# Optimization experiments

Hardware: AMD Instinct MI355X
Metric: run time of the kernel (lower is better)

Reference implementation:

```python
import jax, jax.numpy as jnp
import numpy as np

N = 1500                 # number of proposals
NUM_CLASSES = 81         # COCO: background + 80
NMS_THRESH = 0.5
SCORE_THRESH = 0.05
MAX_DET = 100            # config.test.max_det
BBOX_REG_WEIGHTS = jnp.array([10.0, 10.0, 5.0, 5.0], dtype=jnp.float32)


def setup_inputs() -> dict:
    key = jax.random.key(0)
    k1, k2, k3 = jax.random.split(key, 3)
    H, W = 800.0, 1333.0
    # realistic proposals: random centers / sizes inside the image
    cx = jax.random.uniform(jax.random.fold_in(k1, 0), (N,)) * W
    cy = jax.random.uniform(jax.random.fold_in(k1, 1), (N,)) * H
    bw = jax.random.uniform(jax.random.fold_in(k1, 2), (N,)) * 200.0 + 16.0
    bh = jax.random.uniform(jax.random.fold_in(k1, 3), (N,)) * 200.0 + 16.0
    bottom_rois = jnp.stack(
        [jnp.zeros((N,)), cx - 0.5 * bw, cy - 0.5 * bh, cx + 0.5 * bw, cy + 0.5 * bh],
        axis=1).astype(jnp.float32)
    bbox_delta = (jax.random.normal(k2, (N, 4 * NUM_CLASSES)) * 0.5).astype(jnp.float32)
    cls_prob = jax.nn.softmax(jax.random.normal(k3, (N, NUM_CLASSES)) * 2.0, axis=-1).astype(jnp.float32)
    im_info = jnp.array([[H, W, 1.0]], dtype=jnp.float32)
    return {"bottom_rois": bottom_rois, "bbox_delta": bbox_delta,
            "cls_prob": cls_prob, "im_info": im_info}


def _decode_boxes(rois, deltas, im_info):
    # rois [N,4], deltas [N,4C] -> clipped boxes [N,C,4] (legacy +1 convention)
    x1, y1, x2, y2 = rois[:, 0], rois[:, 1], rois[:, 2], rois[:, 3]
    w = x2 - x1 + 1.0
    h = y2 - y1 + 1.0
    cx = x1 + 0.5 * w
    cy = y1 + 0.5 * h
    d = deltas.reshape(deltas.shape[0], -1, 4) / BBOX_REG_WEIGHTS  # [N,C,4]
    pcx = cx[:, None] + w[:, None] * d[..., 0]
    pcy = cy[:, None] + h[:, None] * d[..., 1]
    pw = w[:, None] * jnp.exp(d[..., 2])
    ph = h[:, None] * jnp.exp(d[..., 3])
    boxes = jnp.stack([pcx - 0.5 * pw, pcy - 0.5 * ph,
                       pcx + 0.5 * pw - 1.0, pcy + 0.5 * ph - 1.0], axis=-1)
    hw = im_info[0, :2]  # [height, width]
    lim = jnp.stack([hw[1] - 1.0, hw[0] - 1.0, hw[1] - 1.0, hw[0] - 1.0])
    return jnp.clip(boxes, 0.0, lim)


def _pairwise_iou(b):
    # b [N,4], legacy +1 areas (matches gpu_nms)
    x1, y1, x2, y2 = b[:, 0], b[:, 1], b[:, 2], b[:, 3]
    area = (x2 - x1 + 1.0) * (y2 - y1 + 1.0)
    iw = jnp.maximum(jnp.minimum(x2[:, None], x2[None, :]) - jnp.maximum(x1[:, None], x1[None, :]) + 1.0, 0.0)
    ih = jnp.maximum(jnp.minimum(y2[:, None], y2[None, :]) - jnp.maximum(y1[:, None], y1[None, :]) + 1.0, 0.0)
    inter = iw * ih
    return inter / (area[:, None] + area[None, :] - inter)


def _nms_one_class(boxes, scores):
    # boxes [N,4], scores [N] -> score-sorted boxes/scores + keep mask
    valid = scores > SCORE_THRESH
    order = jnp.argsort(-scores)
    b = boxes[order]
    s = scores[order]
    v = valid[order]
    iou = jax.lax.stop_gradient(_pairwise_iou(b))  # used only in comparisons

    def body(suppressed, i):
        keep_i = v[i] & ~suppressed[i]
        suppressed = suppressed | (keep_i & (iou[i] > NMS_THRESH))
        return suppressed, keep_i

    _, keep = jax.lax.scan(body, jnp.zeros((b.shape[0],), bool), jnp.arange(b.shape[0]))
    return b, s, keep


def reference(bottom_rois, bbox_delta, cls_prob, im_info):
    boxes = _decode_boxes(bottom_rois[:, 1:], bbox_delta, im_info)  # [N,C,4]
    C = cls_prob.shape[1]
    boxes_fg = jnp.swapaxes(boxes, 0, 1)[1:]   # [C-1,N,4]
    scores_fg = cls_prob.T[1:]                 # [C-1,N]
    b, s, keep = jax.vmap(_nms_one_class)(boxes_fg, scores_fg)
    # image-level max_det cap (>= kth score, as in source)
    flat = jnp.where(keep, s, -jnp.inf).reshape(-1)
    n_keep = keep.sum()
    kth = jax.lax.top_k(flat, MAX_DET)[0][-1]
    keep = keep & jnp.where(n_keep > MAX_DET, s >= kth, True)
    cls_idx = jnp.broadcast_to(jnp.arange(1, C)[:, None], s.shape)
    zeros = jnp.zeros_like(s[..., None])
    dets = jnp.concatenate([zeros, b, s[..., None]], axis=-1)  # [C-1,N,6]
    dets = jnp.where(keep[..., None], dets, 0.0).reshape(-1, 6)
    return dets, cls_idx.reshape(-1), keep.reshape(-1)
```

## Files before the change

kernel.cpp:

```cpp
#include <hip/hip_runtime.h>
#include <math.h>

#pragma clang fp contract(off)

#define N_ROIS     1500
#define NUM_CLS    81
#define FG         80
#define MAXC       1536
#define NMS_T      0.5f
#define SCORE_T    0.05f
#define MAX_DET    100
#define TOTAL      (FG * N_ROIS)
#define TPB        256
#define LDS_STAGE  12288

__device__ __forceinline__ unsigned f2s(float f) {
    unsigned u = __float_as_uint(f);
    return (u & 0x80000000u) ? ~u : (u | 0x80000000u);
}
__device__ __forceinline__ float s2f(unsigned u) {
    return __uint_as_float((u & 0x80000000u) ? (u & 0x7FFFFFFFu) : ~u);
}

__global__ __launch_bounds__(TPB) void nms_kernel(
    const float* __restrict__ rois,
    const float* __restrict__ deltas,
    const float* __restrict__ prob,
    const float* __restrict__ iminfo,
    float4* __restrict__ keptBox,
    int*    __restrict__ keptRow,
    float*  __restrict__ keptScore,
    int*    __restrict__ counter,
    float*  __restrict__ out)
{
    __shared__ unsigned long long key[MAXC];
    __shared__ unsigned long long skey[MAXC];
    __shared__ float4 box4[MAXC];
    __shared__ unsigned char keepf[MAXC], supp[MAXC];
    __shared__ int mcnt;

    const int tid = threadIdx.x;
    const int c = blockIdx.x + 1;
    const int cbase = blockIdx.x * N_ROIS;

    if (tid == 0) mcnt = 0;
    __syncthreads();

    for (int i = tid; i < N_ROIS; i += TPB) {
        float s = prob[i * NUM_CLS + c];
        if (s > SCORE_T) {
            int p = atomicAdd(&mcnt, 1);
            key[p] = ((unsigned long long)(~f2s(s)) << 32) | (unsigned)i;
        }
    }

    {
        const float4 z4 = make_float4(0.f, 0.f, 0.f, 0.f);
        float4* dets4 = (float4*)(out + (size_t)cbase * 6);
        for (int i = tid; i < N_ROIS * 6 / 4; i += TPB) dets4[i] = z4;
        const float fc = (float)c;
        const float4 c4 = make_float4(fc, fc, fc, fc);
        float4* cls4  = (float4*)(out + (size_t)TOTAL * 6 + cbase);
        float4* keep4 = (float4*)(out + (size_t)TOTAL * 7 + cbase);
        for (int i = tid; i < N_ROIS / 4; i += TPB) { cls4[i] = c4; keep4[i] = z4; }
    }
    __syncthreads();
    const int M = mcnt;
    if (M == 0) return;

    for (int i = tid; i < M; i += TPB) {
        unsigned long long kk = key[i];
        int cnt = 0;
        #pragma unroll 4
        for (int j = 0; j < M; ++j) cnt += (int)(key[j] < kk);
        skey[cnt] = kk;
    }
    __syncthreads();

    const float Hm1 = iminfo[0] - 1.0f;
    const float Wm1 = iminfo[1] - 1.0f;
    for (int k = tid; k < M; k += TPB) {
        unsigned long long kk = skey[k];
        int i = (int)(kk & 0xFFFFFFFFu);
        const float* rp = rois + i * 5;
        float x1 = rp[1], y1 = rp[2], x2 = rp[3], y2 = rp[4];
        float w  = x2 - x1 + 1.0f;
        float h  = y2 - y1 + 1.0f;
        float cx = x1 + 0.5f * w;
        float cy = y1 + 0.5f * h;
        const float* dp = deltas + i * (4 * NUM_CLS) + c * 4;
        float dx = dp[0] / 10.0f, dy = dp[1] / 10.0f;
        float dw = dp[2] / 5.0f,  dh = dp[3] / 5.0f;
        float pcx = cx + w * dx;
        float pcy = cy + h * dy;
        float pw  = w * expf(dw);
        float ph  = h * expf(dh);
        float a1 = pcx - 0.5f * pw;
        float a2 = pcy - 0.5f * ph;
        float a3 = pcx + 0.5f * pw - 1.0f;
        float a4 = pcy + 0.5f * ph - 1.0f;
        a1 = fminf(fmaxf(a1, 0.0f), Wm1);
        a2 = fminf(fmaxf(a2, 0.0f), Hm1);
        a3 = fminf(fmaxf(a3, 0.0f), Wm1);
        a4 = fminf(fmaxf(a4, 0.0f), Hm1);
        box4[k] = make_float4(a1, a2, a3, a4);
        keepf[k] = 0; supp[k] = 0;
    }
    __syncthreads();

    const int MW = (M + 63) >> 6;
    const bool fast = (M * MW <= MAXC);

    if (fast) {
        const int wave = tid >> 6, lane = tid & 63;
        for (int r = wave; r < M; r += TPB / 64) {
            float4 br = box4[r];
            float ar = (br.z - br.x + 1.0f) * (br.w - br.y + 1.0f);
            for (int w = 0; w < MW; ++w) {
                int col = (w << 6) | lane;
                int j = col < M ? col : M - 1;
                float4 bj = box4[j];
                float aj = (bj.z - bj.x + 1.0f) * (bj.w - bj.y + 1.0f);
                float iw = fminf(br.z, bj.z) - fmaxf(br.x, bj.x) + 1.0f;
                float ih = fminf(br.w, bj.w) - fmaxf(br.y, bj.y) + 1.0f;
                iw = fmaxf(iw, 0.0f);
                ih = fmaxf(ih, 0.0f);
                float inter = iw * ih;
                float iou = inter / ((ar + aj) - inter);
                bool pred = (col > r) && (col < M) && (iou > NMS_T);
                unsigned long long m = __ballot(pred);
                if (lane == 0) key[r * MW + w] = m;
            }
        }
        __syncthreads();

        if (tid < 64) {
            const int lw = (tid < MW) ? tid : 0;
            unsigned long long acc = 0;
            for (int k = 0; k < M; ++k) {
                unsigned long long m = key[k * MW + lw];
                int bit = (int)((acc >> (k & 63)) & 1ull);
                int sup = __shfl(bit, k >> 6, 64);
                if (!sup) {
                    acc |= m;
                    if (tid == 0) keepf[k] = 1;
                }
            }
        }
        __syncthreads();
    } else {
        for (int k = 0; k < M; ++k) {
            if (!supp[k]) {
                if (tid == 0) keepf[k] = 1;
                float4 bk = box4[k];
                float ak = (bk.z - bk.x + 1.0f) * (bk.w - bk.y + 1.0f);
                for (int j = k + 1 + tid; j < M; j += TPB) {
                    float4 bj = box4[j];
                    float aj = (bj.z - bj.x + 1.0f) * (bj.w - bj.y + 1.0f);
                    float iw = fminf(bk.z, bj.z) - fmaxf(bk.x, bj.x) + 1.0f;
                    float ih = fminf(bk.w, bj.w) - fmaxf(bk.y, bj.y) + 1.0f;
                    iw = fmaxf(iw, 0.0f);
                    ih = fmaxf(ih, 0.0f);
                    float inter = iw * ih;
                    float iou = inter / ((ak + aj) - inter);
                    if (iou > NMS_T) supp[j] = 1;
                }
            }
            __syncthreads();
        }
    }

    for (int k = tid; k < M; k += TPB) {
        if (keepf[k]) {
            int p = atomicAdd(counter, 1);
            keptRow[p]   = cbase + k;
            keptBox[p]   = box4[k];
            keptScore[p] = s2f(~(unsigned)(skey[k] >> 32));
        }
    }
}

__global__ __launch_bounds__(1024) void topk_scatter(
    const int*    __restrict__ counter,
    const int*    __restrict__ keptRow,
    const float4* __restrict__ keptBox,
    const float*  __restrict__ keptScore,
    float* __restrict__ out)
{
    __shared__ unsigned sbits[LDS_STAGE];
    __shared__ int hist[256];
    __shared__ int gsum[64];
    __shared__ unsigned s_pref;
    __shared__ int s_kk;

    const int tid = threadIdx.x;
    const int n = *counter;
    const bool filt = (n > MAX_DET);
    float kth = -INFINITY;

    if (filt) {
        const bool useLds = (n <= LDS_STAGE);
        if (useLds)
            for (int i = tid; i < n; i += 1024) sbits[i] = f2s(keptScore[i]);
        if (tid == 0) { s_pref = 0u; s_kk = MAX_DET; }
        __syncthreads();
        for (int d = 0; d < 4; ++d) {
            const int shift = 24 - 8 * d;
            if (tid < 256) hist[tid] = 0;
            __syncthreads();
            const unsigned pref = s_pref;
            for (int i = tid; i < n; i += 1024) {
                unsigned u = useLds ? sbits[i] : f2s(keptScore[i]);
                if (d == 0 || (u >> (shift + 8)) == pref)
                    atomicAdd(&hist[(u >> shift) & 255u], 1);
            }
            __syncthreads();
            if (tid < 64) {
                int g = tid;
                gsum[g] = hist[4*g] + hist[4*g+1] + hist[4*g+2] + hist[4*g+3];
            }
            if (tid == 0) {
                int kk = s_kk;
                int acc = 0;
                int g = 63;
                for (; g > 0; --g) {
                    int gs = gsum[g];
                    if (acc + gs >= kk) break;
                    acc += gs;
                }
                int v = 4 * g + 3;
                for (; v > 4 * g; --v) {
                    int h = hist[v];
                    if (acc + h >= kk) break;
                    acc += h;
                }
                s_pref = (pref << 8) | (unsigned)v;
                s_kk = kk - acc;
            }
            __syncthreads();
        }
        kth = s2f(s_pref);
    }

    for (int i = tid; i < n; i += 1024) {
        float s = keptScore[i];
        if (!filt || s >= kth) {
            int r = keptRow[i];
            float4 b4 = keptBox[i];
            float* dst = out + (size_t)r * 6;
            dst[1] = b4.x; dst[2] = b4.y; dst[3] = b4.z; dst[4] = b4.w; dst[5] = s;
            out[(size_t)TOTAL * 7 + r] = 1.0f;
        }
    }
}

extern "C" void kernel_launch(void* const* d_in, const int* in_sizes, int n_in,
                              void* d_out, int out_size, void* d_ws, size_t ws_size,
                              hipStream_t stream) {
    const float* rois   = (const float*)d_in[0];
    const float* deltas = (const float*)d_in[1];
    const float* prob   = (const float*)d_in[2];
    const float* iminfo = (const float*)d_in[3];
    float* out = (float*)d_out;

    float4* keptBox   = (float4*)d_ws;
    int*    keptRow   = (int*)(keptBox + TOTAL);
    float*  keptScore = (float*)(keptRow + TOTAL);
    int*    counter   = (int*)(keptScore + TOTAL);

    hipMemsetAsync(counter, 0, sizeof(int), stream);
    nms_kernel<<<FG, TPB, 0, stream>>>(rois, deltas, prob, iminfo,
                                       keptBox, keptRow, keptScore, counter, out);
    topk_scatter<<<1, 1024, 0, stream>>>(counter, keptRow, keptBox, keptScore, out);
}
```

Before: 108.9 us.

## Fuse top-k scatter into NMS kernel via last-block-done counter

Merges the separate single-block top-k/scatter kernel into the NMS kernel: each block bumps an arrival counter after a threadfence, and the last block to arrive runs the radix-select and scatter with 256 threads, reusing the key LDS buffer for staging. It also compacts the score-threshold filter with wave ballot/popcount so there is one LDS atomic per wave instead of per element, and precomputes box areas in LDS. The aim is to remove a kernel launch and its inter-kernel gap. In exchange the serial tail runs with 4x fewer threads, and a smaller LDS staging limit can push large kept counts onto the global-memory path.

```diff
diff --git a/kernel.cpp b/kernel.cpp
--- a/kernel.cpp
+++ b/kernel.cpp
@@ -12,7 +12,6 @@
 #define MAX_DET    100
 #define TOTAL      (FG * N_ROIS)
 #define TPB        256
-#define LDS_STAGE  12288
 
 __device__ __forceinline__ unsigned f2s(float f) {
     unsigned u = __float_as_uint(f);
@@ -22,7 +21,7 @@
     return __uint_as_float((u & 0x80000000u) ? (u & 0x7FFFFFFFu) : ~u);
 }
 
-__global__ __launch_bounds__(TPB) void nms_kernel(
+__global__ __launch_bounds__(TPB) void nms_fused(
     const float* __restrict__ rois,
     const float* __restrict__ deltas,
     const float* __restrict__ prob,
@@ -30,27 +29,40 @@
     float4* __restrict__ keptBox,
     int*    __restrict__ keptRow,
     float*  __restrict__ keptScore,
-    int*    __restrict__ counter,
+    int*    __restrict__ ctrs,
     float*  __restrict__ out)
 {
     __shared__ unsigned long long key[MAXC];
     __shared__ unsigned long long skey[MAXC];
     __shared__ float4 box4[MAXC];
+    __shared__ float  areaA[MAXC];
     __shared__ unsigned char keepf[MAXC], supp[MAXC];
-    __shared__ int mcnt;
-
-    const int tid = threadIdx.x;
+    __shared__ int hist[256];
+    __shared__ int gsum[64];
+    __shared__ unsigned s_pref;
+    __shared__ int s_kk;
+    __shared__ int mcnt, s_arr;
+
+    const int tid  = threadIdx.x;
+    const int lane = tid & 63;
     const int c = blockIdx.x + 1;
     const int cbase = blockIdx.x * N_ROIS;
 
     if (tid == 0) mcnt = 0;
     __syncthreads();
 
-    for (int i = tid; i < N_ROIS; i += TPB) {
-        float s = prob[i * NUM_CLS + c];
-        if (s > SCORE_T) {
-            int p = atomicAdd(&mcnt, 1);
-            key[p] = ((unsigned long long)(~f2s(s)) << 32) | (unsigned)i;
+    for (int i0 = 0; i0 < N_ROIS; i0 += TPB) {
+        int i = i0 + tid;
+        float s = 0.0f;
+        bool val = false;
+        if (i < N_ROIS) { s = prob[i * NUM_CLS + c]; val = (s > SCORE_T); }
+        unsigned long long m = __ballot(val);
+        int base = 0;
+        if (lane == 0 && m) base = atomicAdd(&mcnt, __popcll(m));
+        base = __shfl(base, 0, 64);
+        if (val) {
+            int pos = base + __popcll(m & ((1ull << lane) - 1ull));
+            key[pos] = ((unsigned long long)(~f2s(s)) << 32) | (unsigned)i;
         }
     }
 
@@ -66,142 +78,137 @@
     }
     __syncthreads();
     const int M = mcnt;
-    if (M == 0) return;
-
-    for (int i = tid; i < M; i += TPB) {
-        unsigned long long kk = key[i];
-        int cnt = 0;
-        #pragma unroll 4
-        for (int j = 0; j < M; ++j) cnt += (int)(key[j] < kk);
-        skey[cnt] = kk;
-    }
-    __syncthreads();
-
-    const float Hm1 = iminfo[0] - 1.0f;
-    const float Wm1 = iminfo[1] - 1.0f;
-    for (int k = tid; k < M; k += TPB) {
-        unsigned long long kk = skey[k];
-        int i = (int)(kk & 0xFFFFFFFFu);
-        const float* rp = rois + i * 5;
-        float x1 = rp[1], y1 = rp[2], x2 = rp[3], y2 = rp[4];
-        float w  = x2 - x1 + 1.0f;
-        float h  = y2 - y1 + 1.0f;
-        float cx = x1 + 0.5f * w;
-        float cy = y1 + 0.5f * h;
-        const float* dp = deltas + i * (4 * NUM_CLS) + c * 4;
-        float dx = dp[0] / 10.0f, dy = dp[1] / 10.0f;
-        float dw = dp[2] / 5.0f,  dh = dp[3] / 5.0f;
-        float pcx = cx + w * dx;
-        float pcy = cy + h * dy;
-        float pw  = w * expf(dw);
-        float ph  = h * expf(dh);
-        float a1 = pcx - 0.5f * pw;
-        float a2 = pcy - 0.5f * ph;
-        float a3 = pcx + 0.5f * pw - 1.0f;
-        float a4 = pcy + 0.5f * ph - 1.0f;
-        a1 = fminf(fmaxf(a1, 0.0f), Wm1);
-        a2 = fminf(fmaxf(a2, 0.0f), Hm1);
-        a3 = fminf(fmaxf(a3, 0.0f), Wm1);
-        a4 = fminf(fmaxf(a4, 0.0f), Hm1);
-        box4[k] = make_float4(a1, a2, a3, a4);
-        keepf[k] = 0; supp[k] = 0;
-    }
-    __syncthreads();
-
-    const int MW = (M + 63) >> 6;
-    const bool fast = (M * MW <= MAXC);
-
-    if (fast) {
-        const int wave = tid >> 6, lane = tid & 63;
-        for (int r = wave; r < M; r += TPB / 64) {
-            float4 br = box4[r];
-            float ar = (br.z - br.x + 1.0f) * (br.w - br.y + 1.0f);
-            for (int w = 0; w < MW; ++w) {
-                int col = (w << 6) | lane;
-                int j = col < M ? col : M - 1;
-                float4 bj = box4[j];
-                float aj = (bj.z - bj.x + 1.0f) * (bj.w - bj.y + 1.0f);
-                float iw = fminf(br.z, bj.z) - fmaxf(br.x, bj.x) + 1.0f;
-                float ih = fminf(br.w, bj.w) - fmaxf(br.y, bj.y) + 1.0f;
-                iw = fmaxf(iw, 0.0f);
-                ih = fmaxf(ih, 0.0f);
-                float inter = iw * ih;
-                float iou = inter / ((ar + aj) - inter);
-                bool pred = (col > r) && (col < M) && (iou > NMS_T);
-                unsigned long long m = __ballot(pred);
-                if (lane == 0) key[r * MW + w] = m;
-            }
+
+    if (M > 0) {
+        for (int i = tid; i < M; i += TPB) {
+            unsigned long long kk = key[i];
+            int cnt = 0;
+            #pragma unroll 4
+            for (int j = 0; j < M; ++j) cnt += (int)(key[j] < kk);
+            skey[cnt] = kk;
         }
         __syncthreads();
 
-        if (tid < 64) {
-            const int lw = (tid < MW) ? tid : 0;
-            unsigned long long acc = 0;
-            for (int k = 0; k < M; ++k) {
-                unsigned long long m = key[k * MW + lw];
-                int bit = (int)((acc >> (k & 63)) & 1ull);
-                int sup = __shfl(bit, k >> 6, 64);
-                if (!sup) {
-                    acc |= m;
-                    if (tid == 0) keepf[k] = 1;
-                }
-            }
+        const float Hm1 = iminfo[0] - 1.0f;
+        const float Wm1 = iminfo[1] - 1.0f;
+        for (int k = tid; k < M; k += TPB) {
+            unsigned long long kk = skey[k];
+            int i = (int)(kk & 0xFFFFFFFFu);
+            const float* rp = rois + i * 5;
+            float x1 = rp[1], y1 = rp[2], x2 = rp[3], y2 = rp[4];
+            float w  = x2 - x1 + 1.0f;
+            float h  = y2 - y1 + 1.0f;
+            float cx = x1 + 0.5f * w;
+            float cy = y1 + 0.5f * h;
+            const float* dp = deltas + i * (4 * NUM_CLS) + c * 4;
+            float dx = dp[0] / 10.0f, dy = dp[1] / 10.0f;
+            float dw = dp[2] / 5.0f,  dh = dp[3] / 5.0f;
+            float pcx = cx + w * dx;
+            float pcy = cy + h * dy;
+            float pw  = w * expf(dw);
+            float ph  = h * expf(dh);
+            float a1 = pcx - 0.5f * pw;
+            float a2 = pcy - 0.5f * ph;
+            float a3 = pcx + 0.5f * pw - 1.0f;
+            float a4 = pcy + 0.5f * ph - 1.0f;
+            a1 = fminf(fmaxf(a1, 0.0f), Wm1);
+            a2 = fminf(fmaxf(a2, 0.0f), Hm1);
+            a3 = fminf(fmaxf(a3, 0.0f), Wm1);
+            a4 = fminf(fmaxf(a4, 0.0f), Hm1);
+            box4[k]  = make_float4(a1, a2, a3, a4);
+            areaA[k] = (a3 - a1 + 1.0f) * (a4 - a2 + 1.0f);
+            keepf[k] = 0; supp[k] = 0;
         }
         __syncthreads();
-    } else {
-        for (int k = 0; k < M; ++k) {
-            if (!supp[k]) {
-                if (tid == 0) keepf[k] = 1;
-                float4 bk = box4[k];
-                float ak = (bk.z - bk.x + 1.0f) * (bk.w - bk.y + 1.0f);
-                for (int j = k + 1 + tid; j < M; j += TPB) {
+
+        const int MW = (M + 63) >> 6;
+        const bool fast = (M * MW <= MAXC);
+
+        if (fast) {
+            const int wv = tid >> 6;
+            for (int r = wv; r < M; r += TPB / 64) {
+                float4 br = box4[r];
+                float  ar = areaA[r];
+                for (int w = 0; w < MW; ++w) {
+                    int col = (w << 6) | lane;
+                    bool inb = (col < M);
+                    int j = inb ? col : 0;
                     float4 bj = box4[j];
-                    float aj = (bj.z - bj.x + 1.0f) * (bj.w - bj.y + 1.0f);
-                    float iw = fminf(bk.z, bj.z) - fmaxf(bk.x, bj.x) + 1.0f;
-                    float ih = fminf(bk.w, bj.w) - fmaxf(bk.y, bj.y) + 1.0f;
+                    float  aj = areaA[j];
+                    float iw = fminf(br.z, bj.z) - fmaxf(br.x, bj.x) + 1.0f;
+                    float ih = fminf(br.w, bj.w) - fmaxf(br.y, bj.y) + 1.0f;
                     iw = fmaxf(iw, 0.0f);
                     ih = fmaxf(ih, 0.0f);
                     float inter = iw * ih;
-                    float iou = inter / ((ak + aj) - inter);
-                    if (iou > NMS_T) supp[j] = 1;
-                }
-            }
-            __syncthreads();
-        }
-    }
-
-    for (int k = tid; k < M; k += TPB) {
-        if (keepf[k]) {
-            int p = atomicAdd(counter, 1);
-            keptRow[p]   = cbase + k;
-            keptBox[p]   = box4[k];
-            keptScore[p] = s2f(~(unsigned)(skey[k] >> 32));
-        }
-    }
-}
-
-__global__ __launch_bounds__(1024) void topk_scatter(
-    const int*    __restrict__ counter,
-    const int*    __restrict__ keptRow,
-    const float4* __restrict__ keptBox,
-    const float*  __restrict__ keptScore,
-    float* __restrict__ out)
-{
-    __shared__ unsigned sbits[LDS_STAGE];
-    __shared__ int hist[256];
-    __shared__ int gsum[64];
-    __shared__ unsigned s_pref;
-    __shared__ int s_kk;
-
-    const int tid = threadIdx.x;
-    const int n = *counter;
+                    float iou = inter / ((ar + aj) - inter);
+                    bool pred = inb && (col > r) && (iou > NMS_T);
+                    unsigned long long mk = __ballot(pred);
+                    if (lane == 0) key[r * MW + w] = mk;
+                }
+            }
+            __syncthreads();
+
+            if (tid < 64) {
+                const int lw = (tid < MW) ? tid : 0;
+                unsigned long long acc = 0;
+                for (int k = 0; k < M; ++k) {
+                    unsigned long long m = key[k * MW + lw];
+                    int bit = (int)((acc >> (k & 63)) & 1ull);
+                    int sup = __shfl(bit, k >> 6, 64);
+                    if (!sup) {
+                        acc |= m;
+                        if (tid == 0) keepf[k] = 1;
+                    }
+                }
+            }
+            __syncthreads();
+        } else {
+            for (int k = 0; k < M; ++k) {
+                if (!supp[k]) {
+                    if (tid == 0) keepf[k] = 1;
+                    float4 bk = box4[k];
+                    float  ak = areaA[k];
+                    for (int j = k + 1 + tid; j < M; j += TPB) {
+                        float4 bj = box4[j];
+                        float  aj = areaA[j];
+                        float iw = fminf(bk.z, bj.z) - fmaxf(bk.x, bj.x) + 1.0f;
+                        float ih = fminf(bk.w, bj.w) - fmaxf(bk.y, bj.y) + 1.0f;
+                        iw = fmaxf(iw, 0.0f);
+                        ih = fmaxf(ih, 0.0f);
+                        float inter = iw * ih;
+                        float iou = inter / ((ak + aj) - inter);
+                        if (iou > NMS_T) supp[j] = 1;
+                    }
+                }
+                __syncthreads();
+            }
+        }
+
+        for (int k = tid; k < M; k += TPB) {
+            if (keepf[k]) {
+                int p = atomicAdd(&ctrs[0], 1);
+                keptRow[p]   = cbase + k;
+                keptBox[p]   = box4[k];
+                keptScore[p] = s2f(~(unsigned)(skey[k] >> 32));
+            }
+        }
+    }
+
+    __threadfence();
+    if (tid == 0) s_arr = atomicAdd(&ctrs[1], 1);
+    __syncthreads();
+    if (s_arr != FG - 1) return;
+    __threadfence();
+
+    const int n = ctrs[0];
     const bool filt = (n > MAX_DET);
     float kth = -INFINITY;
 
     if (filt) {
-        const bool useLds = (n <= LDS_STAGE);
+        unsigned* sbits = (unsigned*)key;
+        const bool useLds = (n <= 2 * MAXC);
         if (useLds)
-            for (int i = tid; i < n; i += 1024) sbits[i] = f2s(keptScore[i]);
+            for (int i = tid; i < n; i += TPB) sbits[i] = f2s(keptScore[i]);
         if (tid == 0) { s_pref = 0u; s_kk = MAX_DET; }
         __syncthreads();
         for (int d = 0; d < 4; ++d) {
@@ -209,7 +216,7 @@
             if (tid < 256) hist[tid] = 0;
             __syncthreads();
             const unsigned pref = s_pref;
-            for (int i = tid; i < n; i += 1024) {
+            for (int i = tid; i < n; i += TPB) {
                 unsigned u = useLds ? sbits[i] : f2s(keptScore[i]);
                 if (d == 0 || (u >> (shift + 8)) == pref)
                     atomicAdd(&hist[(u >> shift) & 255u], 1);
@@ -242,7 +249,7 @@
         kth = s2f(s_pref);
     }
 
-    for (int i = tid; i < n; i += 1024) {
+    for (int i = tid; i < n; i += TPB) {
         float s = keptScore[i];
         if (!filt || s >= kth) {
             int r = keptRow[i];
@@ -266,10 +273,9 @@
     float4* keptBox   = (float4*)d_ws;
     int*    keptRow   = (int*)(keptBox + TOTAL);
     float*  keptScore = (float*)(keptRow + TOTAL);
-    int*    counter   = (int*)(keptScore + TOTAL);
-
-    hipMemsetAsync(counter, 0, sizeof(int), stream);
-    nms_kernel<<<FG, TPB, 0, stream>>>(rois, deltas, prob, iminfo,
-                                       keptBox, keptRow, keptScore, counter, out);
-    topk_scatter<<<1, 1024, 0, stream>>>(counter, keptRow, keptBox, keptScore, out);
-}
+    int*    ctrs      = (int*)(keptScore + TOTAL);
+
+    hipMemsetAsync(ctrs, 0, 2 * sizeof(int), stream);
+    nms_fused<<<FG, TPB, 0, stream>>>(rois, deltas, prob, iminfo,
+                                      keptBox, keptRow, keptScore, ctrs, out);
+}
```

After: 123.4 us. +13.4%, slower.
